# Optimization experiments

Hardware: AMD Instinct MI355X
Metric: run time of the kernel (lower is better)

Reference implementation:

```python
import jax, jax.numpy as jnp
import numpy as np

IH, IW = 32, 32
HEADS = 8
DIM_HEAD = 32
INNER = HEADS * DIM_HEAD  # 256
INP = 256
OUP = 256
SCALE = DIM_HEAD ** -0.5


def _relative_index(ih, iw):
    # Reproduce the torch buffer computation (meshgrid indexing='ij').
    yy, xx = np.meshgrid(np.arange(ih), np.arange(iw), indexing='ij')
    coords = np.stack([yy.ravel(), xx.ravel()])            # [2, n]
    rel = coords[:, :, None] - coords[:, None, :]          # [2, n, n]
    rel[0] += ih - 1
    rel[1] += iw - 1
    rel[0] *= 2 * iw - 1
    idx = rel.sum(0).ravel()                               # [n*n]
    return jnp.asarray(idx, dtype=jnp.int32)


def setup_inputs() -> dict:
    key = jax.random.key(0)
    k1, k2, k3, k4 = jax.random.split(key, 4)
    B, N = 16, IH * IW
    x = jax.random.normal(k1, (B, N, INP), dtype=jnp.float32)
    # Parameters (stored as [in, out] so forward is x @ W).
    W_qkv = jax.random.normal(k2, (INP, 3 * INNER), dtype=jnp.float32) * 0.02
    W_out = jax.random.normal(k3, (INNER, OUP), dtype=jnp.float32) * 0.02
    b_out = jnp.zeros((OUP,), dtype=jnp.float32)
    bias_table = jax.random.normal(k4, ((2 * IH - 1) * (2 * IW - 1), HEADS), dtype=jnp.float32) * 0.02
    rel_index = _relative_index(IH, IW)
    return {"x": x, "W_qkv": W_qkv, "W_out": W_out, "b_out": b_out,
            "bias_table": bias_table, "rel_index": rel_index}


def reference(x, W_qkv, W_out, b_out, bias_table, rel_index):
    B, N, _ = x.shape
    qkv = x @ W_qkv                                        # [B, N, 3*inner]
    q, k, v = jnp.split(qkv, 3, axis=-1)
    def to_heads(t):  # b n (h d) -> b h n d
        return t.reshape(B, N, HEADS, DIM_HEAD).transpose(0, 2, 1, 3)
    q, k, v = to_heads(q), to_heads(k), to_heads(v)
    dots = jnp.einsum('bhnd,bhmd->bhnm', q, k) * SCALE     # [B, H, N, N]
    # Gather relative position bias: [n*n, heads] -> [1, heads, n, n]
    rel_bias = bias_table[rel_index].reshape(N, N, HEADS).transpose(2, 0, 1)
    dots = dots + rel_bias[None]
    attn = jax.nn.softmax(dots, axis=-1)
    out = jnp.einsum('bhnm,bhmd->bhnd', attn, v)           # [B, H, N, D]
    out = out.transpose(0, 2, 1, 3).reshape(B, N, INNER)   # b n (h d)
    return out @ W_out + b_out
```

## Files before the change

kernel.cpp:

```cpp
#include <hip/hip_runtime.h>
#include <stdint.h>
#include <stddef.h>


typedef _Float16 f16;
typedef __attribute__((ext_vector_type(8))) _Float16 half8;
typedef __attribute__((ext_vector_type(4))) _Float16 half4;
typedef __attribute__((ext_vector_type(2))) __fp16 fp16x2;
typedef __attribute__((ext_vector_type(4))) float f32x4;

#define MFMA16(a, b, c) __builtin_amdgcn_mfma_f32_16x16x32_f16((a), (b), (c), 0, 0, 0)

__global__ __launch_bounds__(256) void prep_kernel(
    const float* __restrict__ x,
    const float* __restrict__ W_qkv, const float* __restrict__ W_out,
    const float* __restrict__ bias_table,
    f16* __restrict__ Wtq, f16* __restrict__ Wto, f16* __restrict__ ebC,
    f16* __restrict__ xh)
{
  const float kLog2e = 1.4426950408889634f;
  const float kScale = 0.17677669529663687f * kLog2e;
  int tid = blockIdx.x * 256 + threadIdx.x;
  if (tid < 24576) {
    int c = tid >> 5;
    int k8 = (tid & 31) << 3;
    float s = (c < 256) ? kScale : 1.0f;
    f16* dst = Wtq + c * 256 + k8;
#pragma unroll
    for (int j = 0; j < 8; ++j)
      dst[j] = (f16)(W_qkv[(k8 + j) * 768 + c] * s);
  } else if (tid < 32768) {
    int t = tid - 24576;
    int c = t >> 5;
    int k8 = (t & 31) << 3;
    f16* dst = Wto + c * 256 + k8;
#pragma unroll
    for (int j = 0; j < 8; ++j)
      dst[j] = (f16)W_out[(k8 + j) * 256 + c];
  } else if (tid < 97280) {
    int t = tid - 32768;
    int e = t * 8;
    int h = e / 64512;
    int r = e - h * 64512;
    int dy = r >> 10;
    int xi = (r >> 5) & 31;
    int xj0 = r & 31;
    int base = dy * 63 + xi + 31;
    f16* dst = ebC + e;
#pragma unroll
    for (int j = 0; j < 8; ++j)
      dst[j] = (f16)__expf(bias_table[(base - (xj0 + j)) * 8 + h]);
  } else {
    int t = tid - 97280;
    const float* src = x + (size_t)t * 8;
    f16* dst = xh + (size_t)t * 8;
#pragma unroll
    for (int j = 0; j < 8; ++j) dst[j] = (f16)src[j];
  }
}

__global__ __launch_bounds__(256, 4) void qkv_kernel(
    const f16* __restrict__ xh, const f16* __restrict__ Wt,
    f16* __restrict__ Qh, f16* __restrict__ Kh, f16* __restrict__ Vt)
{
  __shared__ f16 Bs[64 * 256];
  int mt = blockIdx.x, nt = blockIdx.y;
  int tid = threadIdx.x;
  int wave = tid >> 6, lane = tid & 63;
  int g = lane >> 4, q16 = lane & 15;
  int cbase = nt * 64;
  char* BsB = (char*)Bs;
  const f16* WtG = Wt + (size_t)cbase * 256;
#pragma unroll
  for (int i = 0; i < 8; ++i) {
    int c = i * 256 + tid;
    int row = c >> 5;
    int colb = (c & 31) << 4;
    half8 v = *(const half8*)(WtG + c * 8);
    *(half8*)(BsB + row * 512 + (colb ^ ((row & 7) << 4))) = v;
  }
  __syncthreads();

  int rbase = mt * 128 + wave * 32;
  const f16* xr0 = xh + (size_t)(rbase + q16) * 256 + g * 8;
  f32x4 acc[2][4] = {};
#pragma unroll 2
  for (int kc = 0; kc < 8; ++kc) {
    half8 bf[4];
#pragma unroll
    for (int cf = 0; cf < 4; ++cf) {
      int row = cf * 16 + q16;
      int colb = kc * 64 + g * 16;
      bf[cf] = *(const half8*)(BsB + row * 512 + (colb ^ ((row & 7) << 4)));
    }
#pragma unroll
    for (int mf = 0; mf < 2; ++mf) {
      half8 af = *(const half8*)(xr0 + (size_t)(mf * 16) * 256 + kc * 32);
#pragma unroll
      for (int cf = 0; cf < 4; ++cf)
        acc[mf][cf] = MFMA16(af, bf[cf], acc[mf][cf]);
    }
  }

#pragma unroll
  for (int mf = 0; mf < 2; ++mf) {
#pragma unroll
    for (int cf = 0; cf < 4; ++cf) {
      int c = cbase + cf * 16 + q16;
      int which = c >> 8, h = (c >> 5) & 7, d = c & 31;
      int m0 = rbase + mf * 16 + g * 4;
      int b = m0 >> 10, n0 = m0 & 1023;
      size_t bh = (size_t)(b * 8 + h);
      if (which == 2) {
        half4 vv;
#pragma unroll
        for (int r = 0; r < 4; ++r) vv[r] = (f16)acc[mf][cf][r];
        *(half4*)(Vt + (((bh << 5) | d) << 10) + n0) = vv;
      } else {
        f16* base = (which == 0) ? Qh : Kh;
#pragma unroll
        for (int r = 0; r < 4; ++r)
          base[((bh << 10) | (n0 + r)) * 32 + d] = (f16)acc[mf][cf][r];
      }
    }
  }
}

__global__ __launch_bounds__(512) void attn_out_kernel(
    const f16* __restrict__ Qh, const f16* __restrict__ Kh,
    const f16* __restrict__ Vt, const f16* __restrict__ ebC,
    const f16* __restrict__ Wto, const float* __restrict__ b_out,
    float* __restrict__ out)
{
  __shared__ f16 Os[8 * 64 * 32];
  int bid = blockIdx.x;
  int b = bid & 15;
  int qt = bid >> 4;
  int wave = threadIdx.x >> 6, lane = threadIdx.x & 63;
  int g = lane >> 4, q16 = lane & 15;
  int h = wave;
  int bh = b * 8 + h;
  int qbase = qt * 64;
  const f16* Qb = Qh + ((size_t)bh << 15);
  const f16* Kb = Kh + ((size_t)bh << 15);
  const f16* Vb = Vt + ((size_t)bh << 15);

  half8 qf0 = *(const half8*)(Qb + (size_t)(qbase +  0 + q16) * 32 + g * 8);
  half8 qf1 = *(const half8*)(Qb + (size_t)(qbase + 16 + q16) * 32 + g * 8);
  half8 qf2 = *(const half8*)(Qb + (size_t)(qbase + 32 + q16) * 32 + g * 8);
  half8 qf3 = *(const half8*)(Qb + (size_t)(qbase + 48 + q16) * 32 + g * 8);

  int kr0 = ((q16 >> 2) << 3) | (q16 & 3);
  const f16* Kp0 = Kb + kr0 * 32 + g * 8;
  const f16* Kp1 = Kp0 + 4 * 32;
  const f16* Vp0 = Vb + (size_t)q16 * 1024 + g * 8;
  const f16* Vp1 = Vb + (size_t)(16 + q16) * 1024 + g * 8;
  int yi0 = qbase >> 5;
  const f16* Bp = ebC + ((((h * 63 + yi0 + 31) * 32 + q16) << 5) + g * 8);

  f32x4 o0a = {0.f,0.f,0.f,0.f}, o1a = {0.f,0.f,0.f,0.f};
  f32x4 o0b = {0.f,0.f,0.f,0.f}, o1b = {0.f,0.f,0.f,0.f};
  f32x4 o0c = {0.f,0.f,0.f,0.f}, o1c = {0.f,0.f,0.f,0.f};
  f32x4 o0d = {0.f,0.f,0.f,0.f}, o1d = {0.f,0.f,0.f,0.f};
  float lsa = 0.f, lsb = 0.f, lsc = 0.f, lsd = 0.f;
  const fp16x2 one2 = {(__fp16)1.0f, (__fp16)1.0f};
  (void)one2;

#if __has_builtin(__builtin_amdgcn_fdot2)
#define LSUM(LS, PU)                                                         \
    LS = __builtin_amdgcn_fdot2(PU.h2[0], one2, LS, false);                  \
    LS = __builtin_amdgcn_fdot2(PU.h2[1], one2, LS, false);                  \
    LS = __builtin_amdgcn_fdot2(PU.h2[2], one2, LS, false);                  \
    LS = __builtin_amdgcn_fdot2(PU.h2[3], one2, LS, false);
#else
#define LSUM(LS, PU)                                                         \
    _Pragma("unroll") for (int i = 0; i < 8; ++i) { LS += (float)PU.h8[i]; }
#endif

#define FRAG_BODY(QF, K0, K1, V0, V1, EB, O0, O1, LS)                        \
  {                                                                          \
    const f32x4 zz = {0.f, 0.f, 0.f, 0.f};                                   \
    f32x4 s0 = MFMA16(K0, QF, zz);              \
    f32x4 s1 = MFMA16(K1, QF, zz);                         \
    union { fp16x2 h2[4]; half8 h8; } pu, eu;                                \
    eu.h8 = EB;                                                              \
    pu.h2[0] = __builtin_amdgcn_cvt_pkrtz(                                   \
        __builtin_amdgcn_exp2f(s0[0]), __builtin_amdgcn_exp2f(s0[1]));       \
    pu.h2[1] = __builtin_amdgcn_cvt_pkrtz(                                   \
        __builtin_amdgcn_exp2f(s0[2]), __builtin_amdgcn_exp2f(s0[3]));       \
    pu.h2[2] = __builtin_amdgcn_cvt_pkrtz(                                   \
        __builtin_amdgcn_exp2f(s1[0]), __builtin_amdgcn_exp2f(s1[1]));       \
    pu.h2[3] = __builtin_amdgcn_cvt_pkrtz(                                   \
        __builtin_amdgcn_exp2f(s1[2]), __builtin_amdgcn_exp2f(s1[3]));       \
    pu.h2[0] *= eu.h2[0];  pu.h2[1] *= eu.h2[1];           \
    pu.h2[2] *= eu.h2[2];  pu.h2[3] *= eu.h2[3];                             \
    LSUM(LS, pu)                                                             \
    O0 = MFMA16(V0, pu.h8, O0);                          \
    O1 = MFMA16(V1, pu.h8, O1);                       \
  }

  half8 kA0 = *(const half8*)Kp0;
  half8 kA1 = *(const half8*)Kp1;
  half8 vA0 = *(const half8*)Vp0;
  half8 vA1 = *(const half8*)Vp1;
  half8 bA0 = *(const half8*)(Bp);
  half8 bA1 = *(const half8*)(Bp + 512);
  half8 bA2 = *(const half8*)(Bp + 1024);
  half8 bA3 = *(const half8*)(Bp + 1536);

  for (int kt = 0; kt < 31; ++kt) {
    size_t ko = (size_t)(kt + 1) * 1024;
    int    co = (kt + 1) * 32;
    const f16* Bn = Bp - ko;
    half8 kB0 = *(const half8*)(Kp0 + ko);
    half8 kB1 = *(const half8*)(Kp1 + ko);
    half8 vB0 = *(const half8*)(Vp0 + co);
    half8 vB1 = *(const half8*)(Vp1 + co);
    half8 bB0 = *(const half8*)(Bn);
    half8 bB1 = *(const half8*)(Bn + 512);
    half8 bB2 = *(const half8*)(Bn + 1024);
    half8 bB3 = *(const half8*)(Bn + 1536);
    __builtin_amdgcn_sched_barrier(0);
    FRAG_BODY(qf0, kA0, kA1, vA0, vA1, bA0, o0a, o1a, lsa);
    FRAG_BODY(qf1, kA0, kA1, vA0, vA1, bA1, o0b, o1b, lsb);
    FRAG_BODY(qf2, kA0, kA1, vA0, vA1, bA2, o0c, o1c, lsc);
    FRAG_BODY(qf3, kA0, kA1, vA0, vA1, bA3, o0d, o1d, lsd);
    kA0 = kB0; kA1 = kB1; vA0 = vB0; vA1 = vB1;
    bA0 = bB0; bA1 = bB1; bA2 = bB2; bA3 = bB3;
  }
  FRAG_BODY(qf0, kA0, kA1, vA0, vA1, bA0, o0a, o1a, lsa);
  FRAG_BODY(qf1, kA0, kA1, vA0, vA1, bA1, o0b, o1b, lsb);
  FRAG_BODY(qf2, kA0, kA1, vA0, vA1, bA2, o0c, o1c, lsc);
  FRAG_BODY(qf3, kA0, kA1, vA0, vA1, bA3, o0d, o1d, lsd);
#undef FRAG_BODY
#undef LSUM

  char* OsB = (char*)Os + h * 4096;
#define FRAG_OUT(O0, O1, LS, F)                                              \
  {                                                                          \
    float l = LS;                                                            \
    l += __shfl_xor(l, 16);                                                  \
    l += __shfl_xor(l, 32);                                                  \
    float invl = 1.0f / l;                                                   \
    int floc = (F) * 16 + q16;                                               \
    int swz = (floc & 7) << 4;                                               \
    half4 w0, w1;                                                            \
    _Pragma("unroll") for (int r = 0; r < 4; ++r) {                          \
      w0[r] = (f16)(O0[r] * invl); w1[r] = (f16)(O1[r] * invl);              \
    }                                                                        \
    *(half4*)(OsB + ((floc * 64 + g * 8) ^ swz)) = w0;                       \
    *(half4*)(OsB + ((floc * 64 + 32 + g * 8) ^ swz)) = w1;                  \
  }
  FRAG_OUT(o0a, o1a, lsa, 0);
  FRAG_OUT(o0b, o1b, lsb, 1);
  FRAG_OUT(o0c, o1c, lsc, 2);
  FRAG_OUT(o0d, o1d, lsd, 3);
#undef FRAG_OUT

  __syncthreads();

  int cb = wave * 32;
  float bias0 = b_out[cb + q16];
  float bias1 = b_out[cb + 16 + q16];
  f32x4 acc[4][2] = {};
  const char* OsA = (const char*)Os;
#pragma unroll
  for (int kc = 0; kc < 8; ++kc) {
    half8 bf0 = *(const half8*)(Wto + (size_t)(cb + q16) * 256 + kc * 32 + g * 8);
    half8 bf1 = *(const half8*)(Wto + (size_t)(cb + 16 + q16) * 256 + kc * 32 + g * 8);
#pragma unroll
    for (int mf = 0; mf < 4; ++mf) {
      int row = mf * 16 + q16;
      half8 af = *(const half8*)(OsA + kc * 4096 +
                                 ((row * 64 + g * 16) ^ ((row & 7) << 4)));
      acc[mf][0] = MFMA16(af, bf0, acc[mf][0]);
      acc[mf][1] = MFMA16(af, bf1, acc[mf][1]);
    }
  }

#pragma unroll
  for (int mf = 0; mf < 4; ++mf) {
#pragma unroll
    for (int cf = 0; cf < 2; ++cf) {
      int c = cb + cf * 16 + q16;
      float bias = cf ? bias1 : bias0;
#pragma unroll
      for (int r = 0; r < 4; ++r) {
        int mm = (b << 10) + qbase + mf * 16 + g * 4 + r;
        out[(size_t)mm * 256 + c] = acc[mf][cf][r] + bias;
      }
    }
  }
}

extern "C" void kernel_launch(void* const* d_in, const int* in_sizes, int n_in,
                              void* d_out, int out_size, void* d_ws, size_t ws_size,
                              hipStream_t stream) {
  (void)in_sizes; (void)n_in; (void)out_size; (void)ws_size;
  const float* x        = (const float*)d_in[0];
  const float* W_qkv    = (const float*)d_in[1];
  const float* W_out    = (const float*)d_in[2];
  const float* b_out    = (const float*)d_in[3];
  const float* bias_tab = (const float*)d_in[4];
  float* out = (float*)d_out;
  char* ws = (char*)d_ws;

  f16* Qh  = (f16*)(ws);
  f16* Kh  = (f16*)(ws + (size_t)(8u  << 20));
  f16* Vt  = (f16*)(ws + (size_t)(16u << 20));
  f16* ebC = (f16*)(ws + (size_t)(24u << 20));
  f16* xh  = (f16*)(ws + (size_t)(40u << 20));
  f16* Wtq = (f16*)(ws + (size_t)(48u << 20));
  f16* Wto = (f16*)(ws + (size_t)(48u << 20) + 768 * 256 * 2);

  hipLaunchKernelGGL(prep_kernel, dim3(2428), dim3(256), 0, stream,
                     x, W_qkv, W_out, bias_tab, Wtq, Wto, ebC, xh);
  hipLaunchKernelGGL(qkv_kernel, dim3(128, 12), dim3(256), 0, stream,
                     xh, Wtq, Qh, Kh, Vt);
  hipLaunchKernelGGL(attn_out_kernel, dim3(256), dim3(512), 0, stream,
                     Qh, Kh, Vt, ebC, Wto, b_out, out);
}
```

Baseline: 78.09 us.

## Fuse fp32-to-fp16 conversion of x into QKV GEMM with LDS-resident A tile

```diff
diff --git a/kernel.cpp b/kernel.cpp
--- a/kernel.cpp
+++ b/kernel.cpp
@@ -12,11 +12,9 @@
 #define MFMA16(a, b, c) __builtin_amdgcn_mfma_f32_16x16x32_f16((a), (b), (c), 0, 0, 0)
 
 __global__ __launch_bounds__(256) void prep_kernel(
-    const float* __restrict__ x,
     const float* __restrict__ W_qkv, const float* __restrict__ W_out,
     const float* __restrict__ bias_table,
-    f16* __restrict__ Wtq, f16* __restrict__ Wto, f16* __restrict__ ebC,
-    f16* __restrict__ xh)
+    f16* __restrict__ Wtq, f16* __restrict__ Wto, f16* __restrict__ ebC)
 {
   const float kLog2e = 1.4426950408889634f;
   const float kScale = 0.17677669529663687f * kLog2e;
@@ -50,78 +48,97 @@
 #pragma unroll
     for (int j = 0; j < 8; ++j)
       dst[j] = (f16)__expf(bias_table[(base - (xj0 + j)) * 8 + h]);
-  } else {
-    int t = tid - 97280;
-    const float* src = x + (size_t)t * 8;
-    f16* dst = xh + (size_t)t * 8;
-#pragma unroll
-    for (int j = 0; j < 8; ++j) dst[j] = (f16)src[j];
   }
 }
 
-__global__ __launch_bounds__(256, 4) void qkv_kernel(
-    const f16* __restrict__ xh, const f16* __restrict__ Wt,
+__global__ __launch_bounds__(256, 2) void qkv_kernel(
+    const float* __restrict__ x, const f16* __restrict__ Wt,
     f16* __restrict__ Qh, f16* __restrict__ Kh, f16* __restrict__ Vt)
 {
+  __shared__ f16 Xs[64 * 256];
   __shared__ f16 Bs[64 * 256];
-  int mt = blockIdx.x, nt = blockIdx.y;
+  int mt = blockIdx.x;
+  int ch = blockIdx.y;
   int tid = threadIdx.x;
   int wave = tid >> 6, lane = tid & 63;
   int g = lane >> 4, q16 = lane & 15;
-  int cbase = nt * 64;
+  char* XsB = (char*)Xs;
   char* BsB = (char*)Bs;
-  const f16* WtG = Wt + (size_t)cbase * 256;
-#pragma unroll
-  for (int i = 0; i < 8; ++i) {
+
+  const float* xg = x + (size_t)(mt * 64) * 256;
+#pragma unroll
+  for (int i = 0; i < 16; ++i) {
     int c = i * 256 + tid;
-    int row = c >> 5;
-    int colb = (c & 31) << 4;
-    half8 v = *(const half8*)(WtG + c * 8);
-    *(half8*)(BsB + row * 512 + (colb ^ ((row & 7) << 4))) = v;
+    int row = c >> 6;
+    int o8 = (c & 63) * 8;
+    f32x4 v = *(const f32x4*)(xg + (size_t)c * 4);
+    half4 hv;
+#pragma unroll
+    for (int j = 0; j < 4; ++j) hv[j] = (f16)v[j];
+    *(half4*)(XsB + ((row * 512 + o8) ^ ((row & 7) << 4))) = hv;
+  }
+
+  {
+    const f16* WtG = Wt + (size_t)(ch * 384) * 256;
+#pragma unroll
+    for (int i = 0; i < 8; ++i) {
+      int c = i * 256 + tid;
+      int row = c >> 5;
+      int colb = (c & 31) << 4;
+      half8 v = *(const half8*)(WtG + c * 8);
+      *(half8*)(BsB + row * 512 + (colb ^ ((row & 7) << 4))) = v;
+    }
   }
   __syncthreads();
 
-  int rbase = mt * 128 + wave * 32;
-  const f16* xr0 = xh + (size_t)(rbase + q16) * 256 + g * 8;
-  f32x4 acc[2][4] = {};
+  int rbase = mt * 64 + wave * 16;
+  for (int p = 0; p < 6; ++p) {
+    int cbase = ch * 384 + p * 64;
+    f32x4 acc[4] = {};
 #pragma unroll 2
-  for (int kc = 0; kc < 8; ++kc) {
-    half8 bf[4];
-#pragma unroll
-    for (int cf = 0; cf < 4; ++cf) {
-      int row = cf * 16 + q16;
-      int colb = kc * 64 + g * 16;
-      bf[cf] = *(const half8*)(BsB + row * 512 + (colb ^ ((row & 7) << 4)));
-    }
-#pragma unroll
-    for (int mf = 0; mf < 2; ++mf) {
-      half8 af = *(const half8*)(xr0 + (size_t)(mf * 16) * 256 + kc * 32);
-#pragma unroll
-      for (int cf = 0; cf < 4; ++cf)
-        acc[mf][cf] = MFMA16(af, bf[cf], acc[mf][cf]);
-    }
-  }
-
-#pragma unroll
-  for (int mf = 0; mf < 2; ++mf) {
+    for (int kc = 0; kc < 8; ++kc) {
+      int rowA = wave * 16 + q16;
+      half8 af = *(const half8*)(XsB +
+          ((rowA * 512 + kc * 64 + g * 16) ^ ((rowA & 7) << 4)));
+#pragma unroll
+      for (int cf = 0; cf < 4; ++cf) {
+        int row = cf * 16 + q16;
+        int colb = kc * 64 + g * 16;
+        half8 bf = *(const half8*)(BsB + row * 512 + (colb ^ ((row & 7) << 4)));
+        acc[cf] = MFMA16(af, bf, acc[cf]);
+      }
+    }
 #pragma unroll
     for (int cf = 0; cf < 4; ++cf) {
       int c = cbase + cf * 16 + q16;
       int which = c >> 8, h = (c >> 5) & 7, d = c & 31;
-      int m0 = rbase + mf * 16 + g * 4;
+      int m0 = rbase + g * 4;
       int b = m0 >> 10, n0 = m0 & 1023;
       size_t bh = (size_t)(b * 8 + h);
       if (which == 2) {
         half4 vv;
 #pragma unroll
-        for (int r = 0; r < 4; ++r) vv[r] = (f16)acc[mf][cf][r];
+        for (int r = 0; r < 4; ++r) vv[r] = (f16)acc[cf][r];
         *(half4*)(Vt + (((bh << 5) | d) << 10) + n0) = vv;
       } else {
         f16* base = (which == 0) ? Qh : Kh;
 #pragma unroll
         for (int r = 0; r < 4; ++r)
-          base[((bh << 10) | (n0 + r)) * 32 + d] = (f16)acc[mf][cf][r];
+          base[((bh << 10) | (n0 + r)) * 32 + d] = (f16)acc[cf][r];
       }
+    }
+    if (p < 5) {
+      __syncthreads();
+      const f16* WtG = Wt + (size_t)(ch * 384 + (p + 1) * 64) * 256;
+#pragma unroll
+      for (int i = 0; i < 8; ++i) {
+        int c = i * 256 + tid;
+        int row = c >> 5;
+        int colb = (c & 31) << 4;
+        half8 v = *(const half8*)(WtG + c * 8);
+        *(half8*)(BsB + row * 512 + (colb ^ ((row & 7) << 4))) = v;
+      }
+      __syncthreads();
     }
   }
 }
@@ -309,14 +326,13 @@
   f16* Kh  = (f16*)(ws + (size_t)(8u  << 20));
   f16* Vt  = (f16*)(ws + (size_t)(16u << 20));
   f16* ebC = (f16*)(ws + (size_t)(24u << 20));
-  f16* xh  = (f16*)(ws + (size_t)(40u << 20));
   f16* Wtq = (f16*)(ws + (size_t)(48u << 20));
   f16* Wto = (f16*)(ws + (size_t)(48u << 20) + 768 * 256 * 2);
 
-  hipLaunchKernelGGL(prep_kernel, dim3(2428), dim3(256), 0, stream,
-                     x, W_qkv, W_out, bias_tab, Wtq, Wto, ebC, xh);
-  hipLaunchKernelGGL(qkv_kernel, dim3(128, 12), dim3(256), 0, stream,
-                     xh, Wtq, Qh, Kh, Vt);
+  hipLaunchKernelGGL(prep_kernel, dim3(380), dim3(256), 0, stream,
+                     W_qkv, W_out, bias_tab, Wtq, Wto, ebC);
+  hipLaunchKernelGGL(qkv_kernel, dim3(256, 2), dim3(256), 0, stream,
+                     x, Wtq, Qh, Kh, Vt);
   hipLaunchKernelGGL(attn_out_kernel, dim3(256), dim3(512), 0, stream,
                      Qh, Kh, Vt, ebC, Wto, b_out, out);
 }
```

New measurement: 74.50 us (median of 2 runs). 1.05x faster.
